# Kernel tuning notes

Measured on AMD Instinct MI355X. Metric: run time of the kernel, lower is better.

Reference implementation:

```python
import itertools
import jax, jax.numpy as jnp
import numpy as np

# ---- static config (mirrors args) ----
BS = 4; NUM_SEM = 24; C = 4 + NUM_SEM
H_SCREEN = 240; W_SCREEN = 320
FOV = 60.0
RES = 5; Z_RES = 5
MAP_SIZE_CM = 4800 // 2            # global_downscaling = 2
MAP_CELLS = MAP_SIZE_CM // RES     # 480
VR = 100                           # vision_range
AGENT_HEIGHT = 1.55 * 100.0        # cm
MAX_H = int(360 / Z_RES)           # 72
MIN_H = int(-40 / Z_RES)           # -8
MAP_PRED_THR = 1.0; EXP_PRED_THR = 1.0; CAT_PRED_THR = 5.0
SHIFT_X = VR * RES // 2            # 250 cm (shift_loc)
XC = (W_SCREEN - 1.0) / 2.0
ZC = (H_SCREEN - 1.0) / 2.0
FOCAL = (W_SCREEN / 2.0) / float(np.tan(np.deg2rad(FOV / 2.0)))
DEG2RAD = float(np.pi / 180.0)
R2D = 57.29577951308232


def splat_feat_nd(init_grid, feat, coords):
    # init_grid [B,F,D0,D1,D2], feat [B,F,N], coords [B,3,N] in [-1,1]
    B, Fc = init_grid.shape[0], init_grid.shape[1]
    dims = init_grid.shape[2:]
    grid_flat = init_grid.reshape(B, Fc, -1)
    pos_all, wts_all = [], []
    for d in range(len(dims)):
        Dd = dims[d]
        pos = coords[:, d, :] * (Dd / 2.0) + Dd / 2.0   # [B,N]
        fl = jnp.floor(pos)
        pd, wd = [], []
        for off in (0.0, 1.0):
            p = fl + off
            safe = ((p > 0) & (p < Dd)).astype(pos.dtype)
            wd.append((1.0 - jnp.abs(pos - p)) * safe)
            pd.append(p * safe)
        pos_all.append(pd); wts_all.append(wd)
    bidx = jnp.arange(B)[:, None, None]
    fidx = jnp.arange(Fc)[None, :, None]
    for corner in itertools.product((0, 1), repeat=len(dims)):
        index = jnp.zeros_like(pos_all[0][0])
        wts = jnp.ones_like(pos_all[0][0])
        for d in range(len(dims)):
            index = index * dims[d] + pos_all[d][corner[d]]
            wts = wts * wts_all[d][corner[d]]
        idx = index.astype(jnp.int32)[:, None, :]        # [B,1,N]
        grid_flat = grid_flat.at[bidx, fidx, idx].add(feat * wts[:, None, :])
    return jnp.round(grid_flat).reshape(init_grid.shape)


def affine_grid(theta, H, W):
    # align_corners=True base grid; theta [B,2,3] -> grid [B,H,W,2]
    xs = jnp.linspace(-1.0, 1.0, W)
    ys = jnp.linspace(-1.0, 1.0, H)
    gx, gy = jnp.meshgrid(xs, ys)                        # [H,W]
    base = jnp.stack([gx, gy, jnp.ones_like(gx)], axis=-1)
    return jnp.einsum('hwk,bjk->bhwj', base, theta)


def grid_sample(img, grid):
    # bilinear, zero padding, align_corners=True. img [B,C,H,W], grid [B,Ho,Wo,2]
    B, Cc, H, W = img.shape
    ix = (grid[..., 0] + 1.0) * 0.5 * (W - 1)
    iy = (grid[..., 1] + 1.0) * 0.5 * (H - 1)
    x0 = jnp.floor(ix); y0 = jnp.floor(iy)
    x1 = x0 + 1.0; y1 = y0 + 1.0
    wx1 = ix - x0; wx0 = 1.0 - wx1
    wy1 = iy - y0; wy0 = 1.0 - wy1
    bidx = jnp.arange(B)[:, None, None]
    def gather(xi, yi):
        valid = ((xi >= 0) & (xi <= W - 1) & (yi >= 0) & (yi <= H - 1)).astype(img.dtype)
        xc = jnp.clip(xi, 0, W - 1).astype(jnp.int32)
        yc = jnp.clip(yi, 0, H - 1).astype(jnp.int32)
        v = img[bidx, :, yc, xc]                          # [B,Ho,Wo,C]
        return v * valid[..., None]
    out = (gather(x0, y0) * (wx0 * wy0)[..., None]
           + gather(x1, y0) * (wx1 * wy0)[..., None]
           + gather(x0, y1) * (wx0 * wy1)[..., None]
           + gather(x1, y1) * (wx1 * wy1)[..., None])
    return jnp.transpose(out, (0, 3, 1, 2))


def setup_inputs():
    key = jax.random.key(0)
    k1, k2, k3, k4, k5, k6, k7 = jax.random.split(key, 7)
    rgb = jax.random.uniform(k1, (BS, 3, H_SCREEN, W_SCREEN), jnp.float32)
    depth = jax.random.uniform(k2, (BS, 1, H_SCREEN, W_SCREEN), jnp.float32, 50.0, 500.0)  # cm
    seg = jax.random.uniform(k3, (BS, NUM_SEM, H_SCREEN, W_SCREEN), jnp.float32)
    obs = jnp.concatenate([rgb, depth, seg], axis=1)
    pose_obs = jax.random.uniform(k4, (BS, 3), jnp.float32, -0.1, 0.1)
    maps_last = jax.random.uniform(k5, (BS, C, MAP_CELLS, MAP_CELLS), jnp.float32)
    xy = jax.random.uniform(k6, (BS, 2), jnp.float32, 8.0, 16.0)   # meters, inside map
    th = jax.random.uniform(k7, (BS, 1), jnp.float32, -180.0, 180.0)
    poses_last = jnp.concatenate([xy, th], axis=1)
    view_angles = jnp.zeros((BS,), jnp.float32)
    return {"obs": obs, "pose_obs": pose_obs, "maps_last": maps_last,
            "poses_last": poses_last, "view_angles": view_angles, "holding_state": 0}


def _forward(obs, pose_obs, maps_last, poses_last, view_angles):
    bs, c, h, w = obs.shape
    # holding_state == 0 path: mask_err_below = depth < 0
    depth = jnp.where(obs[:, 3] < 0.0, 1e4, obs[:, 3])
    # point cloud from depth (du_scale == 1)
    x_idx = jnp.arange(w, dtype=depth.dtype)
    z_idx = jnp.arange(h - 1, -1, -1).astype(depth.dtype)
    X = (x_idx[None, None, :] - XC) * depth / FOCAL
    Z = (z_idx[None, :, None] - ZC) * depth / FOCAL
    XYZ = jnp.stack([X, depth, Z], axis=-1)              # [bs,h,w,3]
    # camera elevation rotation about x-axis, then add sensor height
    a = view_angles * DEG2RAD
    ca, sa = jnp.cos(a), jnp.sin(a)
    z0 = jnp.zeros_like(ca); o1 = jnp.ones_like(ca)
    Rx = jnp.stack([o1, z0, z0, z0, ca, -sa, z0, sa, ca], -1).reshape(bs, 3, 3)
    XYZ = jnp.einsum('bij,bhwj->bhwi', Rx, XYZ)
    XYZ = XYZ.at[..., 2].add(AGENT_HEIGHT)
    # transform_pose_t with shift_loc: z-rotation by pi/2-pi/2=0, +x shift
    XYZ = XYZ.at[..., 0].add(float(SHIFT_X))
    # normalize to [-1,1] voxel coords
    xy_n = (XYZ[..., :2] / RES - VR // 2.0) / VR * 2.0
    z_n = (XYZ[..., 2] / Z_RES - (MAX_H + MIN_H) // 2.0) / (MAX_H - MIN_H) * 2.0
    coords = jnp.concatenate([xy_n, z_n[..., None]], axis=-1)
    coords = coords.reshape(bs, h * w, 3).transpose(0, 2, 1)            # [bs,3,N]
    feat = jnp.concatenate([jnp.ones((bs, 1, h * w), obs.dtype),
                            obs[:, 4:].reshape(bs, c - 4, h * w)], axis=1)
    init_grid = jnp.zeros((bs, 1 + NUM_SEM, VR, VR, MAX_H - MIN_H), obs.dtype)
    voxels = splat_feat_nd(init_grid, feat, coords).transpose(0, 1, 3, 2, 4)
    min_z = int(15 / Z_RES - MIN_H)
    max_z = int((AGENT_HEIGHT + 1 + 50) / Z_RES - MIN_H)
    agent_height_proj = voxels[..., min_z:max_z].sum(-1)
    all_height_proj = voxels.sum(-1)
    fp_map_pred = jnp.clip(agent_height_proj[:, 0:1] / MAP_PRED_THR, 0.0, 1.0)
    fp_exp_pred = jnp.clip(all_height_proj[:, 0:1] / EXP_PRED_THR, 0.0, 1.0)
    x1 = MAP_CELLS // 2 - VR // 2; x2 = x1 + VR
    y1 = MAP_CELLS // 2; look = VR - 4; y2 = y1 + look
    agent_view = jnp.zeros((bs, c, MAP_CELLS, MAP_CELLS), obs.dtype)
    agent_view = agent_view.at[:, 0:1, y1:y2, x1:x2].set(fp_map_pred[:, :, :look, :])
    agent_view = agent_view.at[:, 1:2, y1:y2, x1:x2].set(fp_exp_pred[:, :, :look, :])
    agent_view = agent_view.at[:, 4:, y1:y2, x1:x2].set(
        jnp.clip(agent_height_proj[:, 1:] / CAT_PRED_THR, 0.0, 1.0)[:, :, :look, :])
    # pose composition (get_new_pose_batch)
    th0 = poses_last[:, 2] / R2D
    ny = poses_last[:, 1] + pose_obs[:, 0] * jnp.sin(th0) + pose_obs[:, 1] * jnp.cos(th0)
    nx = poses_last[:, 0] + pose_obs[:, 0] * jnp.cos(th0) - pose_obs[:, 1] * jnp.sin(th0)
    no = poses_last[:, 2] + pose_obs[:, 2] * R2D
    no = jnp.fmod(no - 180.0, 360.0) + 180.0
    no = jnp.fmod(no + 180.0, 360.0) - 180.0
    current_poses = jnp.stack([nx, ny, no], axis=1)
    st = jax.lax.stop_gradient(current_poses)            # st_pose is .detach()ed
    half = MAP_CELLS // 2
    sx = -(st[:, 0] * 100.0 / RES - half) / half
    sy = -(st[:, 1] * 100.0 / RES - half) / half
    t = (90.0 - st[:, 2]) * DEG2RAD
    ct, s_t = jnp.cos(t), jnp.sin(t)
    zz = jnp.zeros_like(ct); oo = jnp.ones_like(ct)
    theta_rot = jnp.stack([ct, -s_t, zz, s_t, ct, zz], -1).reshape(bs, 2, 3)
    theta_tr = jnp.stack([oo, zz, sx, zz, oo, sy], -1).reshape(bs, 2, 3)
    rot_grid = affine_grid(theta_rot, MAP_CELLS, MAP_CELLS)
    trans_grid = affine_grid(theta_tr, MAP_CELLS, MAP_CELLS)
    rotated = grid_sample(agent_view, rot_grid)
    translated = grid_sample(rotated, trans_grid)
    map_pred = jnp.maximum(maps_last, translated)        # torch.max over stacked pair
    return fp_map_pred, map_pred, current_poses, current_poses


def reference(obs, pose_obs, maps_last, poses_last, view_angles, holding_state):
    # holding_state == 0 path (no object held); branches for 1/2 are host-side numpy.
    return _forward(obs, pose_obs, maps_last, poses_last, view_angles)
```

## Files before the change

kernel.cpp:

```cpp
#include <hip/hip_runtime.h>
#include <math.h>

#define BS 4
#define CC 28
#define NF 25
#define HS 240
#define WSC 320
#define NPIX (HS*WSC)
#define VR 100
#define ZD 80
#define MC 480
#define NCELL (VR*VR)
#define NREC_MAX ((size_t)BS*NPIX*4)

__device__ __forceinline__ float clip01(float v){ return fminf(fmaxf(v, 0.f), 1.f); }

struct Geo {
    float wx[2], wy[2], wz[2];
    int   xi[2], yi[2], zi[2];
    bool  sx[2], sy[2];
};

__device__ __forceinline__ Geo compute_geo(const float* __restrict__ obs,
                                           const float* __restrict__ view_angles,
                                           int b, int pix){
    int j = pix % WSC;
    int i = pix / WSC;
    float depth = obs[((size_t)(b*CC + 3))*NPIX + pix];
    if (depth < 0.f) depth = 10000.f;
    const float FOCAL = 277.12812921102035f;
    float X = ((float)j - 159.5f) * depth / FOCAL;
    float Z = ((float)(HS-1-i) - 119.5f) * depth / FOCAL;
    float a = view_angles[b] * 0.017453292519943295f;
    float ca = cosf(a), sa = sinf(a);
    float Y2 = ca*depth - sa*Z;
    float Z2 = sa*depth + ca*Z + 155.f;
    float X2 = X + 250.f;

    float px = ((X2/5.f - 50.f)/100.f*2.f)*50.f + 50.f;
    float py = ((Y2/5.f - 50.f)/100.f*2.f)*50.f + 50.f;
    float pz = ((Z2/5.f - 32.f)/80.f*2.f)*40.f + 40.f;

    Geo g;
    float fx = floorf(px), fy = floorf(py), fz = floorf(pz);
    {
        float p0 = fx, p1 = fx + 1.f;
        g.sx[0] = (p0 > 0.f) && (p0 < 100.f);
        g.sx[1] = (p1 > 0.f) && (p1 < 100.f);
        g.wx[0] = g.sx[0] ? (1.f - fabsf(px - p0)) : 0.f;
        g.wx[1] = g.sx[1] ? (1.f - fabsf(px - p1)) : 0.f;
        g.xi[0] = g.sx[0] ? (int)p0 : 0;
        g.xi[1] = g.sx[1] ? (int)p1 : 0;
    }
    {
        float p0 = fy, p1 = fy + 1.f;
        g.sy[0] = (p0 > 0.f) && (p0 < 100.f);
        g.sy[1] = (p1 > 0.f) && (p1 < 100.f);
        g.wy[0] = g.sy[0] ? (1.f - fabsf(py - p0)) : 0.f;
        g.wy[1] = g.sy[1] ? (1.f - fabsf(py - p1)) : 0.f;
        g.yi[0] = g.sy[0] ? (int)p0 : 0;
        g.yi[1] = g.sy[1] ? (int)p1 : 0;
    }
    {
        float p0 = fz, p1 = fz + 1.f;
        bool s0 = (p0 > 0.f) && (p0 < 80.f);
        bool s1 = (p1 > 0.f) && (p1 < 80.f);
        g.wz[0] = s0 ? (1.f - fabsf(pz - p0)) : 0.f;
        g.wz[1] = s1 ? (1.f - fabsf(pz - p1)) : 0.f;
        g.zi[0] = s0 ? (int)p0 : 0;
        g.zi[1] = s1 ? (int)p1 : 0;
    }
    return g;
}

__global__ void pose_kernel(const float* __restrict__ pose_obs,
                            const float* __restrict__ poses_last,
                            float* __restrict__ out_p1,
                            float* __restrict__ out_p2,
                            float* __restrict__ params){
    int b = threadIdx.x;
    if (b >= BS) return;
    const float R2D = 57.29577951308232f;
    float th0 = poses_last[b*3+2] / R2D;
    float s0 = sinf(th0), c0 = cosf(th0);
    float ny = poses_last[b*3+1] + pose_obs[b*3+0]*s0 + pose_obs[b*3+1]*c0;
    float nx = poses_last[b*3+0] + pose_obs[b*3+0]*c0 - pose_obs[b*3+1]*s0;
    float no = poses_last[b*3+2] + pose_obs[b*3+2]*R2D;
    no = fmodf(no - 180.f, 360.f) + 180.f;
    no = fmodf(no + 180.f, 360.f) - 180.f;
    out_p1[b*3+0] = nx; out_p1[b*3+1] = ny; out_p1[b*3+2] = no;
    out_p2[b*3+0] = nx; out_p2[b*3+1] = ny; out_p2[b*3+2] = no;
    const float half = 240.f;
    float sx = -(nx*100.f/5.f - half)/half;
    float sy = -(ny*100.f/5.f - half)/half;
    float t = (90.f - no) * 0.017453292519943295f;
    params[b*4+0] = cosf(t);
    params[b*4+1] = sinf(t);
    params[b*4+2] = sx;
    params[b*4+3] = sy;
}

__global__ __launch_bounds__(256)
void prep_kernel(const float* __restrict__ obs,
                 const float* __restrict__ view_angles,
                 int* __restrict__ counts,
                 float* __restrict__ feat){
    __shared__ float sf[6400];
    int t   = threadIdx.x;
    int tid = blockIdx.x * 256 + t;
    int b   = tid / NPIX;
    int pix = tid % NPIX;

    Geo g = compute_geo(obs, view_angles, b, pix);
    #pragma unroll
    for (int cy = 0; cy < 2; ++cy)
    #pragma unroll
    for (int cx = 0; cx < 2; ++cx){
        if (g.sx[cx] && g.sy[cy] && (g.wx[cx]*g.wy[cy] != 0.f))
            atomicAdd(&counts[b*NCELL + g.yi[cy]*VR + g.xi[cx]], 1);
    }

    #pragma unroll 6
    for (int f = 0; f < 24; ++f)
        sf[t*25 + f] = obs[((size_t)(b*CC + 4 + f))*NPIX + pix];
    __syncthreads();
    size_t base = ((size_t)b*NPIX + (size_t)(pix - t)) * 24;
    for (int q = t; q < 6144; q += 256)
        feat[base + q] = sf[q + q/24];
}

__global__ void scan_kernel(const int* __restrict__ counts,
                            int* __restrict__ bases,
                            int* __restrict__ cursor){
    __shared__ int part[1024];
    int t = threadIdx.x;
    const int TOT = BS*NCELL;
    const int CH  = 40;
    int beg = t*CH;
    int s = 0;
    for (int i = 0; i < CH; ++i){
        int idx = beg + i;
        if (idx < TOT) s += counts[idx];
    }
    part[t] = s;
    __syncthreads();
    for (int off = 1; off < 1024; off <<= 1){
        int v = (t >= off) ? part[t-off] : 0;
        __syncthreads();
        part[t] += v;
        __syncthreads();
    }
    int run = (t == 0) ? 0 : part[t-1];
    for (int i = 0; i < CH; ++i){
        int idx = beg + i;
        if (idx < TOT){
            bases[idx]  = run;
            cursor[idx] = run;
            run += counts[idx];
        }
    }
}

__global__ __launch_bounds__(256)
void scatter_kernel(const float* __restrict__ obs,
                    const float* __restrict__ view_angles,
                    int* __restrict__ cursor,
                    uint4* __restrict__ records){
    int tid = blockIdx.x * 256 + threadIdx.x;
    int b   = tid / NPIX;
    int pix = tid % NPIX;
    Geo g = compute_geo(obs, view_angles, b, pix);
    #pragma unroll
    for (int cy = 0; cy < 2; ++cy)
    #pragma unroll
    for (int cx = 0; cx < 2; ++cx){
        float wxy = g.wx[cx] * g.wy[cy];
        if (g.sx[cx] && g.sy[cy] && (wxy != 0.f)){
            int cid = b*NCELL + g.yi[cy]*VR + g.xi[cx];
            int pos = atomicAdd(&cursor[cid], 1);
            float w0 = wxy * g.wz[0];
            float w1 = wxy * g.wz[1];
            unsigned iw = (unsigned)pix | ((unsigned)g.zi[0] << 17)
                                        | ((unsigned)g.zi[1] << 24);
            records[pos] = make_uint4(__float_as_uint(w0), __float_as_uint(w1), iw, 0u);
        }
    }
}

__global__ __launch_bounds__(256)
void accum_kernel(const uint4* __restrict__ records,
                  const float* __restrict__ feat,
                  const int* __restrict__ bases,
                  const int* __restrict__ cursor,
                  float* __restrict__ ahp,
                  float* __restrict__ allp,
                  float* __restrict__ out0){
    __shared__ float col[ZD*NF];
    __shared__ uint4 srec[256];
    __shared__ float pall[200], pag[200];

    int cid = blockIdx.x;
    int b   = cid / NCELL;
    int rest = cid % NCELL;
    int y = rest / VR;
    int x = rest % VR;
    int t = threadIdx.x;

    for (int i = t; i < ZD*NF; i += 256) col[i] = 0.f;

    int start = bases[cid];
    int end   = cursor[cid];

    int r = t / NF;
    int f = t % NF;
    bool act = t < 250;
    const float* feat_b = feat + (size_t)b*NPIX*24;

    for (int cb = start; cb < end; cb += 256){
        int n = end - cb; if (n > 256) n = 256;
        __syncthreads();
        if (t < n) srec[t] = records[cb + t];
        __syncthreads();

        for (int sub = 0; sub < n; sub += 40){
            uint4 R[4];
            float V[4];
            bool  valid[4];
            #pragma unroll
            for (int u = 0; u < 4; ++u){
                int idx = sub + u*10 + r;
                valid[u] = act && (idx < n);
                R[u] = valid[u] ? srec[idx] : make_uint4(0u,0u,0u,0u);
            }
            #pragma unroll
            for (int u = 0; u < 4; ++u){
                V[u] = 1.f;
                if (valid[u] && f != 0){
                    int pix = (int)(R[u].z & 0x1FFFFu);
                    V[u] = feat_b[(size_t)pix*24 + (f-1)];
                }
            }
            #pragma unroll
            for (int u = 0; u < 4; ++u){
                if (valid[u]){
                    float w0 = __uint_as_float(R[u].x);
                    float w1 = __uint_as_float(R[u].y);
                    unsigned iw = R[u].z;
                    int z0 = (int)((iw >> 17) & 0x7Fu);
                    int z1 = (int)((iw >> 24) & 0x7Fu);
                    if (w0 != 0.f) atomicAdd(&col[z0*NF + f], V[u] * w0);
                    if (w1 != 0.f) atomicAdd(&col[z1*NF + f], V[u] * w1);
                }
            }
        }
    }
    __syncthreads();

    if (t < 200){
        int ff = t % NF;
        int gq = t / NF;
        float sall = 0.f, sag = 0.f;
        for (int z = gq*10; z < gq*10 + 10; ++z){
            float rv = rintf(col[z*NF + ff]);
            sall += rv;
            if (z >= 11 && z < 49) sag += rv;
        }
        pall[t] = sall;
        pag[t]  = sag;
    }
    __syncthreads();
    if (t < NF){
        float a = 0.f, s = 0.f;
        #pragma unroll
        for (int gq = 0; gq < 8; ++gq){
            s += pall[gq*NF + t];
            a += pag[gq*NF + t];
        }
        ahp[(((size_t)b*NF + t)*VR + y)*VR + x] = a;
        if (t == 0){
            allp[((size_t)b*VR + y)*VR + x] = s;
            out0[(size_t)b*NCELL + y*VR + x] = clip01(a);
        }
    }
}

__global__ __launch_bounds__(256)
void final_kernel(const float* __restrict__ ahp,
                  const float* __restrict__ allp,
                  const float* __restrict__ params,
                  const float* __restrict__ maps_last,
                  float* __restrict__ out1){
    int tid = blockIdx.x * blockDim.x + threadIdx.x;
    if (tid >= BS*MC*MC) return;
    int w = tid % MC;
    int h = (tid / MC) % MC;
    int b = tid / (MC*MC);

    float ct = params[b*4+0], st = params[b*4+1];
    float sx = params[b*4+2], sy = params[b*4+3];

    float gx = -1.f + 2.f*(float)w/479.f;
    float gy = -1.f + 2.f*(float)h/479.f;
    float ix = (gx + sx + 1.f)*0.5f*479.f;
    float iy = (gy + sy + 1.f)*0.5f*479.f;
    float x0 = floorf(ix), y0 = floorf(iy);
    float wx1 = ix - x0, wx0 = 1.f - wx1;
    float wy1 = iy - y0, wy0 = 1.f - wy1;

    int   offs[16];
    float wt16[16];
    int nz = 0;
    #pragma unroll
    for (int tc = 0; tc < 4; ++tc){
        float txf = (tc & 1) ? x0 + 1.f : x0;
        float tyf = (tc & 2) ? y0 + 1.f : y0;
        float wt  = ((tc & 1) ? wx1 : wx0) * ((tc & 2) ? wy1 : wy0);
        bool validT = (txf >= 0.f) && (txf <= 479.f) && (tyf >= 0.f) && (tyf <= 479.f);
        int txc = (int)fminf(fmaxf(txf, 0.f), 479.f);
        int tyc = (int)fminf(fmaxf(tyf, 0.f), 479.f);

        float gx2 = -1.f + 2.f*(float)txc/479.f;
        float gy2 = -1.f + 2.f*(float)tyc/479.f;
        float rgx = ct*gx2 - st*gy2;
        float rgy = st*gx2 + ct*gy2;
        float ixr = (rgx + 1.f)*0.5f*479.f;
        float iyr = (rgy + 1.f)*0.5f*479.f;
        float rx0 = floorf(ixr), ry0 = floorf(iyr);
        float rwx1 = ixr - rx0, rwx0 = 1.f - rwx1;
        float rwy1 = iyr - ry0, rwy0 = 1.f - rwy1;

        #pragma unroll
        for (int rc = 0; rc < 4; ++rc){
            int id = tc*4 + rc;
            float rxf = (rc & 1) ? rx0 + 1.f : rx0;
            float ryf = (rc & 2) ? ry0 + 1.f : ry0;
            float wr  = ((rc & 1) ? rwx1 : rwx0) * ((rc & 2) ? rwy1 : rwy0);
            bool validR = (rxf >= 0.f) && (rxf <= 479.f) && (ryf >= 0.f) && (ryf <= 479.f);
            int rxc = (int)fminf(fmaxf(rxf, 0.f), 479.f);
            int ryc = (int)fminf(fmaxf(ryf, 0.f), 479.f);
            bool inwin = validT && validR &&
                         (rxc >= 190) && (rxc < 290) && (ryc >= 240) && (ryc < 336);
            float wgt = wt * wr;
            if (inwin && wgt != 0.f){
                offs[id] = (ryc - 240)*VR + (rxc - 190);
                wt16[id] = wgt;
                nz++;
            } else {
                offs[id] = -1;
                wt16[id] = 0.f;
            }
        }
    }

    size_t outBase = (size_t)b*CC*MC*MC + (size_t)h*MC + w;
    if (nz == 0){
        #pragma unroll
        for (int ch = 0; ch < CC; ++ch){
            size_t o = outBase + (size_t)ch*MC*MC;
            out1[o] = fmaxf(maps_last[o], 0.f);
        }
        return;
    }

    const float* ahp_b  = ahp  + (size_t)b*NF*VR*VR;
    const float* allp_b = allp + (size_t)b*VR*VR;
    for (int ch = 0; ch < CC; ++ch){
        float acc = 0.f;
        if (ch != 2 && ch != 3){
            #pragma unroll
            for (int id = 0; id < 16; ++id){
                if (offs[id] >= 0){
                    float v;
                    if (ch == 0)      v = clip01(ahp_b[offs[id]]);
                    else if (ch == 1) v = clip01(allp_b[offs[id]]);
                    else              v = clip01(ahp_b[(size_t)(ch-3)*VR*VR + offs[id]] / 5.f);
                    acc += wt16[id] * v;
                }
            }
        }
        size_t o = outBase + (size_t)ch*MC*MC;
        out1[o] = fmaxf(maps_last[o], acc);
    }
}

extern "C" void kernel_launch(void* const* d_in, const int* in_sizes, int n_in,
                              void* d_out, int out_size, void* d_ws, size_t ws_size,
                              hipStream_t stream){
    const float* obs         = (const float*)d_in[0];
    const float* pose_obs    = (const float*)d_in[1];
    const float* maps_last   = (const float*)d_in[2];
    const float* poses_last  = (const float*)d_in[3];
    const float* view_angles = (const float*)d_in[4];
    float* out = (float*)d_out;

    const size_t OUT0 = (size_t)BS*VR*VR;
    const size_t OUT1 = (size_t)BS*CC*MC*MC;
    float* out0 = out;
    float* out1 = out + OUT0;
    float* out2 = out + OUT0 + OUT1;
    float* out3 = out2 + BS*3;

    const size_t AHP_FLOATS  = (size_t)BS*NF*VR*VR;
    const size_t ALLP_FLOATS = (size_t)BS*VR*VR;
    const size_t NCID        = (size_t)BS*NCELL;
    const size_t FEAT_FLOATS = (size_t)BS*NPIX*24;

    float* ahp    = (float*)d_ws;
    float* allp   = ahp  + AHP_FLOATS;
    float* params = allp + ALLP_FLOATS;
    char*  ws_tail = (char*)(params + 16);
    size_t ws_used_small = (size_t)(ws_tail - (char*)d_ws);

    const size_t BIG_BYTES = NCID*3*4 + 32 + NREC_MAX*16 + FEAT_FLOATS*4;
    char* big;
    if (ws_size >= ws_used_small + BIG_BYTES){
        big = ws_tail;
    } else {
        big = (char*)(out1 + OUT1) - BIG_BYTES;
        big = (char*)((uintptr_t)big & ~(uintptr_t)15);
    }
    int* counts = (int*)big;
    int* bases  = counts + NCID;
    int* cursor = bases  + NCID;
    uint4* records = (uint4*)(((uintptr_t)(cursor + NCID) + 15) & ~(uintptr_t)15);
    float* feat    = (float*)(records + NREC_MAX);

    hipMemsetAsync(counts, 0, NCID*4, stream);
    pose_kernel<<<1, 64, 0, stream>>>(pose_obs, poses_last, out2, out3, params);

    int nblk = (BS*NPIX)/256;
    prep_kernel<<<nblk, 256, 0, stream>>>(obs, view_angles, counts, feat);
    scan_kernel<<<1, 1024, 0, stream>>>(counts, bases, cursor);
    scatter_kernel<<<nblk, 256, 0, stream>>>(obs, view_angles, cursor, records);
    accum_kernel<<<(int)NCID, 256, 0, stream>>>(records, feat, bases, cursor,
                                                ahp, allp, out0);
    final_kernel<<<(BS*MC*MC + 255)/256, 256, 0, stream>>>(ahp, allp, params,
                                                           maps_last, out1);
}
```

Measured before the change: 941.0 us.

## Load-balance accum over cell strips with single-wavefront blocks

The accumulation kernel used to launch one 256-thread block per grid cell, even for the many empty cells. Now the scan kernel splits all cells into 4096 strips of roughly equal record count plus a per-cell weight, and each 64-thread block walks its strip of cells in turn. Records are prefetched into registers one chunk ahead, and the final reduction uses a wave shuffle instead of shared memory and barriers. This cuts launch overhead and idle threads on empty cells, but gives less parallelism inside each cell and adds a serial loop over cells per block.

```diff
diff --git a/kernel.cpp b/kernel.cpp
--- a/kernel.cpp
+++ b/kernel.cpp
@@ -12,6 +12,8 @@
 #define MC 480
 #define NCELL (VR*VR)
 #define NREC_MAX ((size_t)BS*NPIX*4)
+#define NSTRIP 4096
+#define CELL_W 8
 
 __device__ __forceinline__ float clip01(float v){ return fminf(fmaxf(v, 0.f), 1.f); }
 
@@ -131,7 +133,8 @@
 
 __global__ void scan_kernel(const int* __restrict__ counts,
                             int* __restrict__ bases,
-                            int* __restrict__ cursor){
+                            int* __restrict__ cursor,
+                            int* __restrict__ cell_start){
     __shared__ int part[1024];
     int t = threadIdx.x;
     const int TOT = BS*NCELL;
@@ -150,6 +153,7 @@
         part[t] += v;
         __syncthreads();
     }
+    int total = part[1023];
     int run = (t == 0) ? 0 : part[t-1];
     for (int i = 0; i < CH; ++i){
         int idx = beg + i;
@@ -158,6 +162,25 @@
             cursor[idx] = run;
             run += counts[idx];
         }
+    }
+    __syncthreads();
+
+    int totw  = total + CELL_W*TOT;
+    int quota = (totw + NSTRIP - 1) / NSTRIP;
+    if (quota < 1) quota = 1;
+    for (int i = 0; i < CH; ++i){
+        int idx = beg + i;
+        if (idx >= TOT) continue;
+        int g1 = (bases[idx] + CELL_W*idx) / quota;
+        if (g1 > NSTRIP-1) g1 = NSTRIP-1;
+        int g0 = -1;
+        if (idx > 0){
+            g0 = (bases[idx-1] + CELL_W*(idx-1)) / quota;
+            if (g0 > NSTRIP-1) g0 = NSTRIP-1;
+        }
+        for (int gg = g0+1; gg <= g1; ++gg) cell_start[gg] = idx;
+        if (idx == TOT-1)
+            for (int gg = g1+1; gg <= NSTRIP; ++gg) cell_start[gg] = TOT;
     }
 }
 
@@ -187,99 +210,114 @@
     }
 }
 
-__global__ __launch_bounds__(256)
+__global__ __launch_bounds__(64)
 void accum_kernel(const uint4* __restrict__ records,
                   const float* __restrict__ feat,
                   const int* __restrict__ bases,
                   const int* __restrict__ cursor,
+                  const int* __restrict__ cell_start,
                   float* __restrict__ ahp,
                   float* __restrict__ allp,
                   float* __restrict__ out0){
     __shared__ float col[ZD*NF];
-    __shared__ uint4 srec[256];
-    __shared__ float pall[200], pag[200];
-
-    int cid = blockIdx.x;
-    int b   = cid / NCELL;
-    int rest = cid % NCELL;
-    int y = rest / VR;
-    int x = rest % VR;
-    int t = threadIdx.x;
-
-    for (int i = t; i < ZD*NF; i += 256) col[i] = 0.f;
-
-    int start = bases[cid];
-    int end   = cursor[cid];
-
-    int r = t / NF;
-    int f = t % NF;
-    bool act = t < 250;
-    const float* feat_b = feat + (size_t)b*NPIX*24;
-
-    for (int cb = start; cb < end; cb += 256){
-        int n = end - cb; if (n > 256) n = 256;
-        __syncthreads();
-        if (t < n) srec[t] = records[cb + t];
-        __syncthreads();
-
-        for (int sub = 0; sub < n; sub += 40){
-            uint4 R[4];
-            float V[4];
-            bool  valid[4];
-            #pragma unroll
-            for (int u = 0; u < 4; ++u){
-                int idx = sub + u*10 + r;
-                valid[u] = act && (idx < n);
-                R[u] = valid[u] ? srec[idx] : make_uint4(0u,0u,0u,0u);
-            }
-            #pragma unroll
-            for (int u = 0; u < 4; ++u){
-                V[u] = 1.f;
-                if (valid[u] && f != 0){
-                    int pix = (int)(R[u].z & 0x1FFFFu);
-                    V[u] = feat_b[(size_t)pix*24 + (f-1)];
+    __shared__ uint4 srec[64];
+
+    int g  = blockIdx.x;
+    int t  = threadIdx.x;
+    int f  = t & 31;
+    int rr = t >> 5;
+    bool flane = (f < NF);
+
+    int c0 = cell_start[g];
+    int c1 = cell_start[g+1];
+
+    for (int cid = c0; cid < c1; ++cid){
+        int b    = cid / NCELL;
+        int rest = cid - b*NCELL;
+        int y = rest / VR;
+        int x = rest - y*VR;
+        int start = bases[cid];
+        int end   = cursor[cid];
+
+        if (start >= end){
+            if (t < NF)
+                ahp[(((size_t)b*NF + t)*VR + y)*VR + x] = 0.f;
+            if (t == 0){
+                allp[((size_t)b*VR + y)*VR + x] = 0.f;
+                out0[(size_t)b*NCELL + y*VR + x] = 0.f;
+            }
+            continue;
+        }
+
+        const float* feat_b = feat + (size_t)b*NPIX*24;
+
+        float4* col4 = (float4*)col;
+        #pragma unroll
+        for (int i = 0; i < 8; ++i){
+            int idx = t + i*64;
+            if (idx < 500) col4[idx] = make_float4(0.f,0.f,0.f,0.f);
+        }
+
+        int n0 = end - start; if (n0 > 64) n0 = 64;
+        uint4 cur = (t < n0) ? records[start + t] : make_uint4(0u,0u,0u,0u);
+
+        for (int cb = start; cb < end; cb += 64){
+            int n = end - cb; if (n > 64) n = 64;
+            srec[t] = cur;
+            int nb = cb + 64;
+            if (nb < end){
+                int n2 = end - nb; if (n2 > 64) n2 = 64;
+                cur = (t < n2) ? records[nb + t] : make_uint4(0u,0u,0u,0u);
+            }
+            for (int sub = 0; sub < n; sub += 8){
+                uint4 R[4]; float V[4]; bool valid[4];
+                #pragma unroll
+                for (int u = 0; u < 4; ++u){
+                    int idx = sub + 2*u + rr;
+                    valid[u] = flane && (idx < n);
+                    R[u] = valid[u] ? srec[idx] : make_uint4(0u,0u,0u,0u);
                 }
-            }
-            #pragma unroll
-            for (int u = 0; u < 4; ++u){
-                if (valid[u]){
-                    float w0 = __uint_as_float(R[u].x);
-                    float w1 = __uint_as_float(R[u].y);
-                    unsigned iw = R[u].z;
-                    int z0 = (int)((iw >> 17) & 0x7Fu);
-                    int z1 = (int)((iw >> 24) & 0x7Fu);
-                    if (w0 != 0.f) atomicAdd(&col[z0*NF + f], V[u] * w0);
-                    if (w1 != 0.f) atomicAdd(&col[z1*NF + f], V[u] * w1);
+                #pragma unroll
+                for (int u = 0; u < 4; ++u){
+                    V[u] = 1.f;
+                    if (valid[u] && f != 0){
+                        int pix = (int)(R[u].z & 0x1FFFFu);
+                        V[u] = feat_b[(size_t)pix*24 + (f-1)];
+                    }
                 }
-            }
-        }
-    }
-    __syncthreads();
-
-    if (t < 200){
-        int ff = t % NF;
-        int gq = t / NF;
+                #pragma unroll
+                for (int u = 0; u < 4; ++u){
+                    if (valid[u]){
+                        float w0 = __uint_as_float(R[u].x);
+                        float w1 = __uint_as_float(R[u].y);
+                        unsigned iw = R[u].z;
+                        int z0 = (int)((iw >> 17) & 0x7Fu);
+                        int z1 = (int)((iw >> 24) & 0x7Fu);
+                        if (w0 != 0.f) atomicAdd(&col[z0*NF + f], V[u]*w0);
+                        if (w1 != 0.f) atomicAdd(&col[z1*NF + f], V[u]*w1);
+                    }
+                }
+            }
+        }
+
+        int f2 = (t < 50) ? (t % NF) : 0;
+        int q  = (t < 50) ? (t / NF) : 0;
         float sall = 0.f, sag = 0.f;
-        for (int z = gq*10; z < gq*10 + 10; ++z){
-            float rv = rintf(col[z*NF + ff]);
+        for (int z = q*40; z < q*40 + 40; ++z){
+            float rv = rintf(col[z*NF + f2]);
             sall += rv;
             if (z >= 11 && z < 49) sag += rv;
         }
-        pall[t] = sall;
-        pag[t]  = sag;
-    }
-    __syncthreads();
-    if (t < NF){
-        float a = 0.f, s = 0.f;
-        #pragma unroll
-        for (int gq = 0; gq < 8; ++gq){
-            s += pall[gq*NF + t];
-            a += pag[gq*NF + t];
-        }
-        ahp[(((size_t)b*NF + t)*VR + y)*VR + x] = a;
-        if (t == 0){
-            allp[((size_t)b*VR + y)*VR + x] = s;
-            out0[(size_t)b*NCELL + y*VR + x] = clip01(a);
+        float sall_o = __shfl(sall, (t + 25) & 63, 64);
+        float sag_o  = __shfl(sag,  (t + 25) & 63, 64);
+        if (t < NF){
+            float a = sag  + sag_o;
+            float s = sall + sall_o;
+            ahp[(((size_t)b*NF + t)*VR + y)*VR + x] = a;
+            if (t == 0){
+                allp[((size_t)b*VR + y)*VR + x] = s;
+                out0[(size_t)b*NCELL + y*VR + x] = clip01(a);
+            }
         }
     }
 }
@@ -404,6 +442,7 @@
     const size_t ALLP_FLOATS = (size_t)BS*VR*VR;
     const size_t NCID        = (size_t)BS*NCELL;
     const size_t FEAT_FLOATS = (size_t)BS*NPIX*24;
+    const size_t CS_INTS     = NSTRIP + 1;
 
     float* ahp    = (float*)d_ws;
     float* allp   = ahp  + AHP_FLOATS;
@@ -411,7 +450,7 @@
     char*  ws_tail = (char*)(params + 16);
     size_t ws_used_small = (size_t)(ws_tail - (char*)d_ws);
 
-    const size_t BIG_BYTES = NCID*3*4 + 32 + NREC_MAX*16 + FEAT_FLOATS*4;
+    const size_t BIG_BYTES = NCID*3*4 + CS_INTS*4 + 64 + NREC_MAX*16 + FEAT_FLOATS*4;
     char* big;
     if (ws_size >= ws_used_small + BIG_BYTES){
         big = ws_tail;
@@ -419,10 +458,11 @@
         big = (char*)(out1 + OUT1) - BIG_BYTES;
         big = (char*)((uintptr_t)big & ~(uintptr_t)15);
     }
-    int* counts = (int*)big;
-    int* bases  = counts + NCID;
-    int* cursor = bases  + NCID;
-    uint4* records = (uint4*)(((uintptr_t)(cursor + NCID) + 15) & ~(uintptr_t)15);
+    int* counts     = (int*)big;
+    int* bases      = counts + NCID;
+    int* cursor     = bases  + NCID;
+    int* cell_start = cursor + NCID;
+    uint4* records = (uint4*)(((uintptr_t)(cell_start + CS_INTS) + 15) & ~(uintptr_t)15);
     float* feat    = (float*)(records + NREC_MAX);
 
     hipMemsetAsync(counts, 0, NCID*4, stream);
@@ -430,10 +470,10 @@
 
     int nblk = (BS*NPIX)/256;
     prep_kernel<<<nblk, 256, 0, stream>>>(obs, view_angles, counts, feat);
-    scan_kernel<<<1, 1024, 0, stream>>>(counts, bases, cursor);
+    scan_kernel<<<1, 1024, 0, stream>>>(counts, bases, cursor, cell_start);
     scatter_kernel<<<nblk, 256, 0, stream>>>(obs, view_angles, cursor, records);
-    accum_kernel<<<(int)NCID, 256, 0, stream>>>(records, feat, bases, cursor,
-                                                ahp, allp, out0);
+    accum_kernel<<<NSTRIP, 64, 0, stream>>>(records, feat, bases, cursor, cell_start,
+                                            ahp, allp, out0);
     final_kernel<<<(BS*MC*MC + 255)/256, 256, 0, stream>>>(ahp, allp, params,
                                                            maps_last, out1);
 }
```

Result: slower. 1.015 ms (+7.9%).
